# Kernel tuning notes

Measured on AMD Instinct MI355X. Metric: run time of the kernel, lower is better.

The kernel has to match this reference:

```python
import jax, jax.numpy as jnp
import numpy as np

B, N, M, D = 8, 4096, 4096, 128


def _cdist(x, y):
    # Euclidean distance via gram trick (matches torch.cdist p=2 math)
    # x: (B,N,D), y: (B,M,D) -> (B,N,M)
    x2 = jnp.sum(x * x, axis=-1)  # (B,N)
    y2 = jnp.sum(y * y, axis=-1)  # (B,M)
    xy = jnp.einsum('bnd,bmd->bnm', x, y)  # (B,N,M)
    sq = x2[:, :, None] + y2[:, None, :] - 2.0 * xy
    return jnp.sqrt(jnp.maximum(sq, 0.0))


def setup_inputs() -> dict:
    key = jax.random.key(0)
    k1, k2 = jax.random.split(key)
    predicted_set = jax.random.normal(k1, (B, N, D), dtype=jnp.float32)
    target_set = jax.random.normal(k2, (B, M, D), dtype=jnp.float32)
    return {"predicted_set": predicted_set, "target_set": target_set}


def reference(predicted_set, target_set):
    pairwise = _cdist(predicted_set, target_set)       # (B,N,M)
    forward_distance = jnp.min(pairwise, axis=1)        # (B,M)  (min over predicted points)
    backward_distance = jnp.min(pairwise, axis=0)       # (N,M)  (min over BATCH, as in original code)
    # reduction = 'mean'
    return jnp.mean(forward_distance) + jnp.mean(backward_distance)
```

## Files before the change

### kernel.cpp

```cpp
#include <hip/hip_runtime.h>
#include <hip/hip_fp8.h>

#define BB 8
#define NN 4096
#define MM 4096
#define DD 128

typedef float f32x4  __attribute__((ext_vector_type(4)));
typedef float f32x16 __attribute__((ext_vector_type(16)));
typedef int   i32x4  __attribute__((ext_vector_type(4)));
typedef int   i32x8  __attribute__((ext_vector_type(8)));


__global__ __launch_bounds__(256)
void prep_all(const float* __restrict__ x, const float* __restrict__ y,
              unsigned char* __restrict__ xq, unsigned char* __restrict__ yq,
              float* __restrict__ x2, float* __restrict__ y2,
              unsigned int* __restrict__ fwd, float* __restrict__ bsum,
              float* __restrict__ fsum, unsigned int* __restrict__ counter) {
    __shared__ i32x4 lbuf[256];

    const int tid  = threadIdx.x;
    const int g    = blockIdx.x;
    const int gtid = g * 256 + tid;
    if (gtid < BB * MM) fwd[gtid] = 0x7f800000u;
    if (gtid == 0) { *bsum = 0.0f; *fsum = 0.0f; *counter = 0u; }

    const int rl = tid >> 3;
    const int c  = tid & 7;

    const float* src;
    unsigned char* dst;
    float* sq;
    float sgn;
    int row;
    if (g < 1024) {
        src = x; dst = xq + (size_t)g * 4096; sq = x2; sgn = 1.0f;
        row = g * 32 + rl;
    } else {
        src = y; dst = yq + (size_t)(g - 1024) * 4096; sq = y2; sgn = -1.0f;
        row = (g - 1024) * 32 + rl;
    }

    const f32x4* base = (const f32x4*)(src + (size_t)row * DD + c * 16);
    f32x4 v[4];
    #pragma unroll
    for (int j = 0; j < 4; ++j) v[j] = base[j];

    float s = 0.0f;
    #pragma unroll
    for (int j = 0; j < 4; ++j)
        s += v[j].x * v[j].x + v[j].y * v[j].y + v[j].z * v[j].z + v[j].w * v[j].w;

    i32x4 d;
    #pragma unroll
    for (int j = 0; j < 4; ++j) {
        unsigned int dj = (unsigned int)__builtin_amdgcn_cvt_pk_fp8_f32(
            sgn * v[j].x, sgn * v[j].y, 0, false);
        dj = (unsigned int)__builtin_amdgcn_cvt_pk_fp8_f32(
            sgn * v[j].z, sgn * v[j].w, (int)dj, true);
        d[j] = (int)dj;
    }

    const int lds_off = (c >> 2) * 2048 + ((c >> 1) & 1) * 1024
                      + rl * 32 + (c & 1) * 16;
    *(i32x4*)((char*)lbuf + lds_off) = d;

    #pragma unroll
    for (int m = 4; m; m >>= 1) s += __shfl_xor(s, m, 64);
    if (c == 0) sq[row] = 0.5f * s;

    __syncthreads();
    *(i32x4*)(dst + (size_t)tid * 16) = lbuf[tid];
}

__global__ __launch_bounds__(256, 4)
void chamfer_main(const unsigned char* __restrict__ xq, const unsigned char* __restrict__ yq,
                  const float* __restrict__ x2, const float* __restrict__ y2,
                  unsigned int* __restrict__ fwd, float* __restrict__ bpart) {
    __shared__ float x2s[BB][128];
    __shared__ float y2s[BB][32];
    __shared__ unsigned int fbuf[BB][32];
    __shared__ float red[4];

    const int tid   = threadIdx.x;
    const int lane  = tid & 63;
    const int wave  = tid >> 6;
    const int lhalf = lane >> 5;
    const int l31   = lane & 31;

    const int id  = blockIdx.x;
    const int xcd = id & 7;
    const int j   = id >> 3;
    const int nb  = (xcd >> 1) * 8 + (j & 7);
    const int mb  = (xcd & 1) * 64 + (j >> 3);
    const int n0b = nb * 128;
    const int n0w = n0b + wave * 32;
    const int m0  = mb * 32;

    const size_t laneoff = (size_t)lhalf * 1024 + (size_t)l31 * 32;
    const unsigned char* xbase = xq + (size_t)(n0w >> 5) * 4096 + laneoff;
    const unsigned char* ybase = yq + (size_t)mb * 4096 + laneoff;

    for (int i = tid; i < BB * 128; i += 256)
        x2s[i >> 7][i & 127] = x2[(size_t)(i >> 7) * NN + n0b + (i & 127)];
    if (tid < BB * 32) {
        y2s[tid >> 5][tid & 31] = y2[(size_t)(tid >> 5) * MM + m0 + (tid & 31)];
        ((unsigned int*)fbuf)[tid] = 0x7f800000u;
    }
    __syncthreads();

    i32x4 fx[2][2][2], fy[2][2][2];
    auto loadb = [&](int b, int s) {
        const unsigned char* xb = xbase + ((size_t)b << 19);
        const unsigned char* yb = ybase + ((size_t)b << 19);
        #pragma unroll
        for (int i = 0; i < 2; ++i)
            #pragma unroll
            for (int hh = 0; hh < 2; ++hh) {
                fx[s][i][hh] = *(const i32x4*)(xb + i * 2048 + hh * 16);
                fy[s][i][hh] = *(const i32x4*)(yb + i * 2048 + hh * 16);
            }
    };
    loadb(0, 0);

    const float INF = __builtin_inff();
    float bmin[16];
    #pragma unroll
    for (int r = 0; r < 16; ++r) bmin[r] = INF;

    #pragma unroll 2
    for (int b = 0; b < BB; ++b) {
        const int cur = b & 1;
        if (b < BB - 1) loadb(b + 1, cur ^ 1);

        float y2v = y2s[b][l31];
        f32x16 acc;
        #pragma unroll
        for (int q = 0; q < 4; ++q) {
            f32x4 xv = *(const f32x4*)&x2s[b][wave * 32 + lhalf * 4 + q * 8];
            #pragma unroll
            for (int e = 0; e < 4; ++e)
                acc[q * 4 + e] = xv[e] + y2v;
        }

        #pragma unroll
        for (int i = 0; i < 2; ++i) {
            i32x8 av = __builtin_shufflevector(fx[cur][i][0], fx[cur][i][1],
                                               0, 1, 2, 3, 4, 5, 6, 7);
            i32x8 bv = __builtin_shufflevector(fy[cur][i][0], fy[cur][i][1],
                                               0, 1, 2, 3, 4, 5, 6, 7);
            acc = __builtin_amdgcn_mfma_scale_f32_32x32x64_f8f6f4(
                av, bv, acc, 0, 0, 0, 127, 0, 127);
        }

        float fm = INF;
        #pragma unroll
        for (int r = 0; r < 16; ++r) {
            bmin[r] = fminf(bmin[r], acc[r]);
            fm      = fminf(fm, acc[r]);
        }
        atomicMin(&fbuf[b][l31], __float_as_uint(fmaxf(fm, 0.0f)));
    }
    __syncthreads();

    {
        int b = tid >> 5, c = tid & 31;
        atomicMin(&fwd[(size_t)b * MM + m0 + c], fbuf[b][c]);
    }

    float s = 0.0f;
    #pragma unroll
    for (int r = 0; r < 16; ++r)
        s += sqrtf(2.0f * fmaxf(bmin[r], 0.0f));
    #pragma unroll
    for (int off = 32; off; off >>= 1) s += __shfl_down(s, off, 64);
    if (lane == 0) red[wave] = s;
    __syncthreads();
    if (tid == 0) bpart[id] = red[0] + red[1] + red[2] + red[3];
}

__global__ __launch_bounds__(256)
void finalize_kernel(const unsigned int* __restrict__ fwd,
                     const float* __restrict__ bpart,
                     float* __restrict__ bsum, float* __restrict__ fsum,
                     unsigned int* __restrict__ counter, float* __restrict__ out) {
    __shared__ float redf[4], redb[4];
    __shared__ int isLast;
    const int tid = threadIdx.x, lane = tid & 63, wave = tid >> 6;
    const int gtid = blockIdx.x * 256 + tid;
    uint4 u = ((const uint4*)fwd)[gtid];
    float sf = sqrtf(2.0f * __uint_as_float(u.x)) + sqrtf(2.0f * __uint_as_float(u.y)) +
               sqrtf(2.0f * __uint_as_float(u.z)) + sqrtf(2.0f * __uint_as_float(u.w));
    float sb = (gtid < 4096) ? bpart[gtid] : 0.0f;
    #pragma unroll
    for (int off = 32; off; off >>= 1) {
        sf += __shfl_down(sf, off, 64);
        sb += __shfl_down(sb, off, 64);
    }
    if (lane == 0) { redf[wave] = sf; redb[wave] = sb; }
    __syncthreads();
    if (tid == 0) {
        atomicAdd(fsum, redf[0] + redf[1] + redf[2] + redf[3]);
        atomicAdd(bsum, redb[0] + redb[1] + redb[2] + redb[3]);
        __threadfence();
        unsigned int c = atomicAdd(counter, 1u);
        isLast = (c == gridDim.x - 1) ? 1 : 0;
        if (isLast) {
            __threadfence();
            float fs = __hip_atomic_load(fsum, __ATOMIC_RELAXED,
                                         __HIP_MEMORY_SCOPE_AGENT);
            float bs = __hip_atomic_load(bsum, __ATOMIC_RELAXED,
                                         __HIP_MEMORY_SCOPE_AGENT);
            out[0] = fs / (float)(BB * MM) + bs / ((float)NN * (float)MM);
        }
    }
}

extern "C" void kernel_launch(void* const* d_in, const int* in_sizes, int n_in,
                              void* d_out, int out_size, void* d_ws, size_t ws_size,
                              hipStream_t stream) {
    const float* x = (const float*)d_in[0];
    const float* y = (const float*)d_in[1];
    float* out = (float*)d_out;

    char* w = (char*)d_ws;
    unsigned char* xq = (unsigned char*)(w);
    unsigned char* yq = (unsigned char*)(w + 4194304);
    float*    x2 = (float*)(w + 8388608);
    float*    y2 = (float*)(w + 8519680);
    unsigned int* fwd = (unsigned int*)(w + 8650752);
    float*    bpart = (float*)(w + 8781824);
    float*    bsum = (float*)(w + 8798208);
    float*    fsum = (float*)(w + 8798212);
    unsigned int* counter = (unsigned int*)(w + 8798216);

    prep_all<<<2048, 256, 0, stream>>>(x, y, xq, yq, x2, y2,
                                       fwd, bsum, fsum, counter);
    chamfer_main<<<4096, 256, 0, stream>>>(xq, yq, x2, y2, fwd, bpart);
    finalize_kernel<<<32, 256, 0, stream>>>(fwd, bpart, bsum, fsum, counter, out);
}
```

Measured before the change: 126.2 us.

## Widen block tile to 64 columns and stage shared Y fragments in LDS

Each block now covers 128x64 instead of 128x32, so every wave runs two MFMA accumulators per batch and the grid is halved. Y fragments are loaded once per block into double-buffered LDS through global_load_lds and read by all four waves, instead of each wave loading its own copy from global memory. This lowers redundant global/L2 traffic for Y and per-block setup, at the cost of more registers (launch bounds drop to 3 blocks), a __syncthreads per batch iteration, and extra LDS reads.

```diff
diff --git a/kernel.cpp b/kernel.cpp
--- a/kernel.cpp
+++ b/kernel.cpp
@@ -11,6 +11,13 @@
 typedef int   i32x4  __attribute__((ext_vector_type(4)));
 typedef int   i32x8  __attribute__((ext_vector_type(8)));
 
+
+typedef const __attribute__((address_space(1))) unsigned int* gas_ptr;
+typedef __attribute__((address_space(3))) unsigned int* las_ptr;
+static __device__ __forceinline__ void gload_lds16(const unsigned char* g,
+                                                   unsigned char* l) {
+    __builtin_amdgcn_global_load_lds((gas_ptr)g, (las_ptr)l, 16, 0, 0);
+}
 
 __global__ __launch_bounds__(256)
 void prep_all(const float* __restrict__ x, const float* __restrict__ y,
@@ -74,13 +81,14 @@
     *(i32x4*)(dst + (size_t)tid * 16) = lbuf[tid];
 }
 
-__global__ __launch_bounds__(256, 4)
+__global__ __launch_bounds__(256, 3)
 void chamfer_main(const unsigned char* __restrict__ xq, const unsigned char* __restrict__ yq,
                   const float* __restrict__ x2, const float* __restrict__ y2,
                   unsigned int* __restrict__ fwd, float* __restrict__ bpart) {
     __shared__ float x2s[BB][128];
-    __shared__ float y2s[BB][32];
-    __shared__ unsigned int fbuf[BB][32];
+    __shared__ float y2s[BB][64];
+    __shared__ unsigned int fbuf[BB][64];
+    __shared__ unsigned char ybuf[2][8192];
     __shared__ float red[4];
 
     const int tid   = threadIdx.x;
@@ -93,86 +101,114 @@
     const int xcd = id & 7;
     const int j   = id >> 3;
     const int nb  = (xcd >> 1) * 8 + (j & 7);
-    const int mb  = (xcd & 1) * 64 + (j >> 3);
+    const int mb  = (xcd & 1) * 32 + (j >> 3);
     const int n0b = nb * 128;
     const int n0w = n0b + wave * 32;
-    const int m0  = mb * 32;
+    const int m0  = mb * 64;
 
     const size_t laneoff = (size_t)lhalf * 1024 + (size_t)l31 * 32;
     const unsigned char* xbase = xq + (size_t)(n0w >> 5) * 4096 + laneoff;
-    const unsigned char* ybase = yq + (size_t)mb * 4096 + laneoff;
-
+
+    const size_t ysw = (size_t)(wave >> 1) * 2048 + (size_t)(wave & 1) * 1024
+                     + ((size_t)lhalf << 4) + (size_t)l31 * 32;
+    const unsigned char* ybase = yq + (size_t)(2 * mb) * 4096 + ysw;
+    const int rb0 = l31 * 16 + lhalf * 1024;
+
+    auto stage_y = [&](int b, int s) {
+        const unsigned char* gsrc = ybase + ((size_t)b << 19);
+        gload_lds16(gsrc,        &ybuf[s][wave * 1024]);
+        gload_lds16(gsrc + 4096, &ybuf[s][4096 + wave * 1024]);
+    };
+
+    i32x4 fx[2][2][2];
+    auto loadx = [&](int b, int s) {
+        const unsigned char* xb = xbase + ((size_t)b << 19);
+        #pragma unroll
+        for (int i = 0; i < 2; ++i)
+            #pragma unroll
+            for (int hh = 0; hh < 2; ++hh)
+                fx[s][i][hh] = *(const i32x4*)(xb + i * 2048 + hh * 16);
+    };
+
+    stage_y(0, 0);
+    loadx(0, 0);
     for (int i = tid; i < BB * 128; i += 256)
         x2s[i >> 7][i & 127] = x2[(size_t)(i >> 7) * NN + n0b + (i & 127)];
-    if (tid < BB * 32) {
-        y2s[tid >> 5][tid & 31] = y2[(size_t)(tid >> 5) * MM + m0 + (tid & 31)];
-        ((unsigned int*)fbuf)[tid] = 0x7f800000u;
-    }
-    __syncthreads();
-
-    i32x4 fx[2][2][2], fy[2][2][2];
-    auto loadb = [&](int b, int s) {
-        const unsigned char* xb = xbase + ((size_t)b << 19);
-        const unsigned char* yb = ybase + ((size_t)b << 19);
-        #pragma unroll
-        for (int i = 0; i < 2; ++i)
-            #pragma unroll
-            for (int hh = 0; hh < 2; ++hh) {
-                fx[s][i][hh] = *(const i32x4*)(xb + i * 2048 + hh * 16);
-                fy[s][i][hh] = *(const i32x4*)(yb + i * 2048 + hh * 16);
-            }
-    };
-    loadb(0, 0);
+    for (int i = tid; i < BB * 64; i += 256) {
+        y2s[i >> 6][i & 63] = y2[(size_t)(i >> 6) * MM + m0 + (i & 63)];
+        ((unsigned int*)fbuf)[i] = 0x7f800000u;
+    }
+    __syncthreads();
 
     const float INF = __builtin_inff();
-    float bmin[16];
-    #pragma unroll
-    for (int r = 0; r < 16; ++r) bmin[r] = INF;
+    float bmin[2][16];
+    #pragma unroll
+    for (int t = 0; t < 2; ++t)
+        #pragma unroll
+        for (int r = 0; r < 16; ++r) bmin[t][r] = INF;
 
     #pragma unroll 2
     for (int b = 0; b < BB; ++b) {
         const int cur = b & 1;
-        if (b < BB - 1) loadb(b + 1, cur ^ 1);
-
-        float y2v = y2s[b][l31];
-        f32x16 acc;
+        if (b < BB - 1) {
+            stage_y(b + 1, cur ^ 1);
+            loadx(b + 1, cur ^ 1);
+        }
+
+        float y2v[2];
+        y2v[0] = y2s[b][l31];
+        y2v[1] = y2s[b][32 + l31];
+        f32x16 acc[2];
         #pragma unroll
         for (int q = 0; q < 4; ++q) {
             f32x4 xv = *(const f32x4*)&x2s[b][wave * 32 + lhalf * 4 + q * 8];
             #pragma unroll
-            for (int e = 0; e < 4; ++e)
-                acc[q * 4 + e] = xv[e] + y2v;
+            for (int t = 0; t < 2; ++t)
+                #pragma unroll
+                for (int e = 0; e < 4; ++e)
+                    acc[t][q * 4 + e] = xv[e] + y2v[t];
         }
 
         #pragma unroll
         for (int i = 0; i < 2; ++i) {
             i32x8 av = __builtin_shufflevector(fx[cur][i][0], fx[cur][i][1],
                                                0, 1, 2, 3, 4, 5, 6, 7);
-            i32x8 bv = __builtin_shufflevector(fy[cur][i][0], fy[cur][i][1],
-                                               0, 1, 2, 3, 4, 5, 6, 7);
-            acc = __builtin_amdgcn_mfma_scale_f32_32x32x64_f8f6f4(
-                av, bv, acc, 0, 0, 0, 127, 0, 127);
-        }
-
-        float fm = INF;
-        #pragma unroll
-        for (int r = 0; r < 16; ++r) {
-            bmin[r] = fminf(bmin[r], acc[r]);
-            fm      = fminf(fm, acc[r]);
-        }
-        atomicMin(&fbuf[b][l31], __float_as_uint(fmaxf(fm, 0.0f)));
-    }
-    __syncthreads();
-
-    {
-        int b = tid >> 5, c = tid & 31;
-        atomicMin(&fwd[(size_t)b * MM + m0 + c], fbuf[b][c]);
-    }
+            #pragma unroll
+            for (int t = 0; t < 2; ++t) {
+                const unsigned char* yb = &ybuf[cur][t * 4096 + i * 2048 + rb0];
+                i32x4 lo = *(const i32x4*)(yb);
+                i32x4 hi = *(const i32x4*)(yb + 512);
+                i32x8 bv = __builtin_shufflevector(lo, hi, 0, 1, 2, 3, 4, 5, 6, 7);
+                acc[t] = __builtin_amdgcn_mfma_scale_f32_32x32x64_f8f6f4(
+                    av, bv, acc[t], 0, 0, 0, 127, 0, 127);
+            }
+        }
+
+        float fm[2] = {INF, INF};
+        #pragma unroll
+        for (int t = 0; t < 2; ++t)
+            #pragma unroll
+            for (int r = 0; r < 16; ++r) {
+                bmin[t][r] = fminf(bmin[t][r], acc[t][r]);
+                fm[t]      = fminf(fm[t], acc[t][r]);
+            }
+        #pragma unroll
+        for (int t = 0; t < 2; ++t)
+            atomicMin(&fbuf[b][t * 32 + l31],
+                      __float_as_uint(fmaxf(fm[t], 0.0f)));
+
+        __syncthreads();
+    }
+
+    for (int i = tid; i < BB * 64; i += 256)
+        atomicMin(&fwd[(size_t)(i >> 6) * MM + m0 + (i & 63)], fbuf[i >> 6][i & 63]);
 
     float s = 0.0f;
     #pragma unroll
-    for (int r = 0; r < 16; ++r)
-        s += sqrtf(2.0f * fmaxf(bmin[r], 0.0f));
+    for (int t = 0; t < 2; ++t)
+        #pragma unroll
+        for (int r = 0; r < 16; ++r)
+            s += sqrtf(2.0f * fmaxf(bmin[t][r], 0.0f));
     #pragma unroll
     for (int off = 32; off; off >>= 1) s += __shfl_down(s, off, 64);
     if (lane == 0) red[wave] = s;
@@ -192,7 +228,7 @@
     uint4 u = ((const uint4*)fwd)[gtid];
     float sf = sqrtf(2.0f * __uint_as_float(u.x)) + sqrtf(2.0f * __uint_as_float(u.y)) +
                sqrtf(2.0f * __uint_as_float(u.z)) + sqrtf(2.0f * __uint_as_float(u.w));
-    float sb = (gtid < 4096) ? bpart[gtid] : 0.0f;
+    float sb = (gtid < 2048) ? bpart[gtid] : 0.0f;
     #pragma unroll
     for (int off = 32; off; off >>= 1) {
         sf += __shfl_down(sf, off, 64);
@@ -237,6 +273,6 @@
 
     prep_all<<<2048, 256, 0, stream>>>(x, y, xq, yq, x2, y2,
                                        fwd, bsum, fsum, counter);
-    chamfer_main<<<4096, 256, 0, stream>>>(xq, yq, x2, y2, fwd, bpart);
+    chamfer_main<<<2048, 256, 0, stream>>>(xq, yq, x2, y2, fwd, bpart);
     finalize_kernel<<<32, 256, 0, stream>>>(fwd, bpart, bsum, fsum, counter, out);
 }
```

Result: faster. 116.8 us (-7.5%).
